# Kernel optimization log

Hardware: AMD Instinct MI355X
Metric: run time of the kernel (lower is better)

## Reference

```python
import jax, jax.numpy as jnp
import numpy as np
from jax import lax

B, C, H, W = 32, 384, 56, 56


def setup_inputs() -> dict:
    key = jax.random.key(0)
    k1, k2, k3, k4 = jax.random.split(key, 4)
    x = jax.random.normal(k1, (B, C, H, W), dtype=jnp.float32)
    # positional embedding, trunc_normal(std=0.02) ~ small normal
    pe = 0.02 * jax.random.normal(k2, (1, C, H, 1), dtype=jnp.float32)
    # depthwise conv weight: (out=C, in/groups=1, kH=H, kW=1), PyTorch default init scale
    fan_in = H  # in_channels/groups * kH * kW = 1*H*1
    bound = 1.0 / np.sqrt(fan_in)
    weight = jax.random.uniform(k3, (C, 1, H, 1), dtype=jnp.float32, minval=-bound, maxval=bound)
    bias = jax.random.uniform(k4, (C,), dtype=jnp.float32, minval=-bound, maxval=bound)
    return {"x": x, "pe": pe, "weight": weight, "bias": bias}


def reference(x, pe, weight, bias):
    # PE add
    xp = x + pe  # [B,C,H,W]
    # circular pad along H: concat first H-1 rows at the bottom
    x_cat = jnp.concatenate([xp, xp[:, :, : H - 1, :]], axis=2)  # [B,C,2H-1,W]
    # depthwise conv, kernel (H,1), groups=C -> output [B,C,H,W]
    out = lax.conv_general_dilated(
        x_cat, weight,
        window_strides=(1, 1), padding='VALID',
        dimension_numbers=('NCHW', 'OIHW', 'NCHW'),
        feature_group_count=C,
    )
    return out + bias[None, :, None, None]
```

## Files before the change

kernel.cpp:

```cpp
#include <hip/hip_runtime.h>

#define Cc 384
#define Hh 56
#define Ww 56
#define PLANE (Hh*Ww)
#define NF4 14

typedef short short8 __attribute__((ext_vector_type(8)));
typedef float f32x4  __attribute__((ext_vector_type(4)));
typedef unsigned int u32;
struct __align__(16) f4 { float x, y, z, w; };

__device__ __forceinline__ u32 cvtpk_bf16(float a, float b) {
    u32 d; asm("v_cvt_pk_bf16_f32 %0, %1, %2" : "=v"(d) : "v"(a), "v"(b));
    return d;
}
__device__ __forceinline__ int swz(int w) { return (w ^ (w >> 2)) & 7; }

__global__ __launch_bounds__(256) __attribute__((amdgpu_waves_per_eu(4, 4)))
void parc_kernel(const float* __restrict__ x, const float* __restrict__ pe,
                 const float* __restrict__ wgt, const float* __restrict__ bias,
                 float* __restrict__ out)
{
    __shared__ __align__(16) unsigned short Xt16[64 * 64];
    __shared__ __align__(16) float Cb[56 * 60];
    __shared__ unsigned short wt2[112];

    const int t  = threadIdx.x;
    const int bc = blockIdx.x;
    const int c  = bc % Cc;

    const float* __restrict__ wc  = wgt + c * Hh;
    const float* __restrict__ pec = pe  + c * Hh;
    const f4* __restrict__ xin = reinterpret_cast<const f4*>(x) + (size_t)bc * (PLANE / 4);

    f4 v0 = xin[t], v1 = xin[t + 256], v2 = xin[t + 512];
    const int r0 = t / NF4, r1 = (t + 256) / NF4, r2 = (t + 512) / NF4;
    const float p0 = pec[r0], p1 = pec[r1], p2 = pec[r2];
    f4 v3; float p3 = 0.f; int r3 = 0;
    if (t < 16) { v3 = xin[t + 768]; r3 = (t + 768) / NF4; p3 = pec[r3]; }

    if (t < 112) {
        const int k = t >= Hh ? t - Hh : t;
        wt2[t] = (unsigned short)(cvtpk_bf16(wc[k], wc[k]) & 0xffffu);
    }

    {
        const int w = t >> 2, j = t & 3;
        const int blk = 7 ^ swz(w);
        *reinterpret_cast<u32*>((char*)Xt16 + 128 * w + 16 * blk + 4 * j) = 0u;
    }

    #define PUT(F, V, R, P) { \
        const int w4_ = (F) % NF4; \
        const int blkb = (R) >> 3, sub = 2 * ((R) & 7); \
        const unsigned short b0 = (unsigned short)cvtpk_bf16((V).x + (P), 0.f); \
        const unsigned short b1 = (unsigned short)cvtpk_bf16((V).y + (P), 0.f); \
        const unsigned short b2 = (unsigned short)cvtpk_bf16((V).z + (P), 0.f); \
        const unsigned short b3 = (unsigned short)cvtpk_bf16((V).w + (P), 0.f); \
        { const int w = 4 * w4_ + 0; *reinterpret_cast<unsigned short*>((char*)Xt16 + 128*w + 16*(blkb ^ swz(w)) + sub) = b0; } \
        { const int w = 4 * w4_ + 1; *reinterpret_cast<unsigned short*>((char*)Xt16 + 128*w + 16*(blkb ^ swz(w)) + sub) = b1; } \
        { const int w = 4 * w4_ + 2; *reinterpret_cast<unsigned short*>((char*)Xt16 + 128*w + 16*(blkb ^ swz(w)) + sub) = b2; } \
        { const int w = 4 * w4_ + 3; *reinterpret_cast<unsigned short*>((char*)Xt16 + 128*w + 16*(blkb ^ swz(w)) + sub) = b3; } }
    PUT(t,       v0, r0, p0)
    PUT(t + 256, v1, r1, p1)
    PUT(t + 512, v2, r2, p2)
    if (t < 16) PUT(t + 768, v3, r3, p3)
    #undef PUT
    __syncthreads();

    const int l = t & 63, wv = t >> 6, l15 = l & 15, g = l >> 4;

    short8 afr[2];
    #pragma unroll
    for (int step = 0; step < 2; ++step) {
        #pragma unroll
        for (int j = 0; j < 8; ++j) {
            int idx = 32 * step + 8 * g + j - 16 * wv - l15 + 56;
            idx = idx < 0 ? 0 : (idx > 111 ? 111 : idx);
            afr[step][j] = (short)wt2[idx];
        }
    }

    const float bz = bias[c];
    f32x4 acc[4];
    #pragma unroll
    for (int ni = 0; ni < 4; ++ni) acc[ni] = (f32x4){bz, bz, bz, bz};

    #pragma unroll
    for (int step = 0; step < 2; ++step) {
        #pragma unroll
        for (int ni = 0; ni < 4; ++ni) {
            const int w = 16 * ni + l15;
            const int blk0 = g + 4 * step;
            const short8 bfr = *reinterpret_cast<const short8*>(
                (char*)Xt16 + 128 * w + 16 * (blk0 ^ swz(w)));
            acc[ni] = __builtin_amdgcn_mfma_f32_16x16x32_bf16(afr[step], bfr, acc[ni], 0, 0, 0);
        }
    }

    #pragma unroll
    for (int ni = 0; ni < 4; ++ni) {
        const int wcol = 16 * ni + l15;
        #pragma unroll
        for (int r = 0; r < 4; ++r) {
            const int h = 16 * wv + 4 * g + r;
            if (h < Hh && wcol < Ww) Cb[60 * h + wcol] = acc[ni][r];
        }
    }
    __syncthreads();

    f4* __restrict__ op = reinterpret_cast<f4*>(out) + (size_t)bc * (PLANE / 4);
    #define GETST(U) { \
        const int rr = (U) / NF4, ww4 = (U) % NF4; \
        op[(U)] = *reinterpret_cast<const f4*>((char*)Cb + 240 * rr + 16 * ww4); }
    GETST(t)
    GETST(t + 256)
    GETST(t + 512)
    if (t < 16) GETST(t + 768)
    #undef GETST
}

extern "C" void kernel_launch(void* const* d_in, const int* in_sizes, int n_in,
                              void* d_out, int out_size, void* d_ws, size_t ws_size,
                              hipStream_t stream) {
    const float* x  = (const float*)d_in[0];
    const float* pe = (const float*)d_in[1];
    const float* w  = (const float*)d_in[2];
    const float* b  = (const float*)d_in[3];
    float* out      = (float*)d_out;

    parc_kernel<<<dim3(32 * Cc), 256, 0, stream>>>(x, pe, w, b, out);
}
```

Measured before the change: 56.59 us.

## Make kernel persistent over six planes with register-prefetched next-plane loads

Launches 2048 blocks that each loop over six (batch, channel) planes instead of one block per plane. The next plane's x, pe, weight and bias loads are issued into registers before the current plane's MFMA and store phase, and the weight LDS buffer is double-buffered. The goal is to hide global load latency behind compute and stores and to cut per-block launch overhead. In exchange it raises register pressure and adds extra barriers per iteration, with a fixed waves_per_eu of 4.

```diff
diff --git a/kernel.cpp b/kernel.cpp
--- a/kernel.cpp
+++ b/kernel.cpp
@@ -5,6 +5,8 @@
 #define Ww 56
 #define PLANE (Hh*Ww)
 #define NF4 14
+#define NBLK 2048
+#define NPL 6
 
 typedef short short8 __attribute__((ext_vector_type(8)));
 typedef float f32x4  __attribute__((ext_vector_type(4)));
@@ -24,32 +26,33 @@
 {
     __shared__ __align__(16) unsigned short Xt16[64 * 64];
     __shared__ __align__(16) float Cb[56 * 60];
-    __shared__ unsigned short wt2[112];
+    __shared__ unsigned short wt2[2][112];
 
-    const int t  = threadIdx.x;
-    const int bc = blockIdx.x;
-    const int c  = bc % Cc;
+    const int t   = threadIdx.x;
+    const int blk = blockIdx.x;
 
-    const float* __restrict__ wc  = wgt + c * Hh;
-    const float* __restrict__ pec = pe  + c * Hh;
-    const f4* __restrict__ xin = reinterpret_cast<const f4*>(x) + (size_t)bc * (PLANE / 4);
-
-    f4 v0 = xin[t], v1 = xin[t + 256], v2 = xin[t + 512];
-    const int r0 = t / NF4, r1 = (t + 256) / NF4, r2 = (t + 512) / NF4;
-    const float p0 = pec[r0], p1 = pec[r1], p2 = pec[r2];
-    f4 v3; float p3 = 0.f; int r3 = 0;
-    if (t < 16) { v3 = xin[t + 768]; r3 = (t + 768) / NF4; p3 = pec[r3]; }
-
-    if (t < 112) {
-        const int k = t >= Hh ? t - Hh : t;
-        wt2[t] = (unsigned short)(cvtpk_bf16(wc[k], wc[k]) & 0xffffu);
-    }
+    const int r0 = t / NF4, r1 = (t + 256) / NF4, r2 = (t + 512) / NF4, r3 = (t + 768) / NF4;
+    const int kw = t >= Hh ? t - Hh : t;
+    const int l = t & 63, wvi = t >> 6, l15 = l & 15, g = l >> 4;
 
     {
         const int w = t >> 2, j = t & 3;
-        const int blk = 7 ^ swz(w);
-        *reinterpret_cast<u32*>((char*)Xt16 + 128 * w + 16 * blk + 4 * j) = 0u;
+        const int blkz = 7 ^ swz(w);
+        *reinterpret_cast<u32*>((char*)Xt16 + 128 * w + 16 * blkz + 4 * j) = 0u;
     }
+
+    f4 v0, v1, v2, v3 = {};
+    float p0 = 0.f, p1 = 0.f, p2 = 0.f, p3 = 0.f, wld = 0.f, bz = 0.f;
+
+    #define ISSUE(BC) { \
+        const f4* __restrict__ xin = reinterpret_cast<const f4*>(x) + (size_t)(BC) * (PLANE / 4); \
+        const int c_ = (BC) % Cc; \
+        const float* __restrict__ pec = pe + c_ * Hh; \
+        v0 = xin[t]; v1 = xin[t + 256]; v2 = xin[t + 512]; \
+        p0 = pec[r0]; p1 = pec[r1]; p2 = pec[r2]; \
+        if (t < 16) { v3 = xin[t + 768]; p3 = pec[r3]; } \
+        if (t < 112) wld = wgt[c_ * Hh + kw]; \
+        bz = bias[c_]; }
 
     #define PUT(F, V, R, P) { \
         const int w4_ = (F) % NF4; \
@@ -62,63 +65,82 @@
         { const int w = 4 * w4_ + 1; *reinterpret_cast<unsigned short*>((char*)Xt16 + 128*w + 16*(blkb ^ swz(w)) + sub) = b1; } \
         { const int w = 4 * w4_ + 2; *reinterpret_cast<unsigned short*>((char*)Xt16 + 128*w + 16*(blkb ^ swz(w)) + sub) = b2; } \
         { const int w = 4 * w4_ + 3; *reinterpret_cast<unsigned short*>((char*)Xt16 + 128*w + 16*(blkb ^ swz(w)) + sub) = b3; } }
-    PUT(t,       v0, r0, p0)
-    PUT(t + 256, v1, r1, p1)
-    PUT(t + 512, v2, r2, p2)
-    if (t < 16) PUT(t + 768, v3, r3, p3)
-    #undef PUT
+
+    #define SCATTER(PAR) { \
+        if (t < 112) wt2[PAR][t] = (unsigned short)(cvtpk_bf16(wld, wld) & 0xffffu); \
+        PUT(t,       v0, r0, p0) \
+        PUT(t + 256, v1, r1, p1) \
+        PUT(t + 512, v2, r2, p2) \
+        if (t < 16) { PUT(t + 768, v3, r3, p3) } }
+
+    ISSUE(blk)
+    SCATTER(0)
+    float bzc = bz;
     __syncthreads();
 
-    const int l = t & 63, wv = t >> 6, l15 = l & 15, g = l >> 4;
+    for (int it = 0; it < NPL; ++it) {
+        const int par = it & 1;
+        const int bc_cur = blk + NBLK * it;
 
-    short8 afr[2];
-    #pragma unroll
-    for (int step = 0; step < 2; ++step) {
+        short8 afr[2];
         #pragma unroll
-        for (int j = 0; j < 8; ++j) {
-            int idx = 32 * step + 8 * g + j - 16 * wv - l15 + 56;
-            idx = idx < 0 ? 0 : (idx > 111 ? 111 : idx);
-            afr[step][j] = (short)wt2[idx];
+        for (int step = 0; step < 2; ++step) {
+            #pragma unroll
+            for (int j = 0; j < 8; ++j) {
+                int idx = 32 * step + 8 * g + j - 16 * wvi - l15 + 56;
+                idx = idx < 0 ? 0 : (idx > 111 ? 111 : idx);
+                afr[step][j] = (short)wt2[par][idx];
+            }
+        }
+
+        if (it + 1 < NPL) { ISSUE(blk + NBLK * (it + 1)) }
+
+        f32x4 acc[4];
+        #pragma unroll
+        for (int ni = 0; ni < 4; ++ni) acc[ni] = (f32x4){bzc, bzc, bzc, bzc};
+
+        #pragma unroll
+        for (int step = 0; step < 2; ++step) {
+            #pragma unroll
+            for (int ni = 0; ni < 4; ++ni) {
+                const int w = 16 * ni + l15;
+                const int blk0 = g + 4 * step;
+                const short8 bfr = *reinterpret_cast<const short8*>(
+                    (char*)Xt16 + 128 * w + 16 * (blk0 ^ swz(w)));
+                acc[ni] = __builtin_amdgcn_mfma_f32_16x16x32_bf16(afr[step], bfr, acc[ni], 0, 0, 0);
+            }
+        }
+
+        #pragma unroll
+        for (int ni = 0; ni < 4; ++ni) {
+            const int wcol = 16 * ni + l15;
+            #pragma unroll
+            for (int r = 0; r < 4; ++r) {
+                const int h = 16 * wvi + 4 * g + r;
+                if (h < Hh && wcol < Ww) Cb[60 * h + wcol] = acc[ni][r];
+            }
+        }
+        __syncthreads();
+
+        f4* __restrict__ op = reinterpret_cast<f4*>(out) + (size_t)bc_cur * (PLANE / 4);
+        #define GETST(U) { \
+            const int rr = (U) / NF4, ww4 = (U) % NF4; \
+            op[(U)] = *reinterpret_cast<const f4*>((char*)Cb + 240 * rr + 16 * ww4); }
+        GETST(t)
+        GETST(t + 256)
+        GETST(t + 512)
+        if (t < 16) { GETST(t + 768) }
+        #undef GETST
+
+        if (it + 1 < NPL) {
+            SCATTER(par ^ 1)
+            bzc = bz;
+            __syncthreads();
         }
     }
-
-    const float bz = bias[c];
-    f32x4 acc[4];
-    #pragma unroll
-    for (int ni = 0; ni < 4; ++ni) acc[ni] = (f32x4){bz, bz, bz, bz};
-
-    #pragma unroll
-    for (int step = 0; step < 2; ++step) {
-        #pragma unroll
-        for (int ni = 0; ni < 4; ++ni) {
-            const int w = 16 * ni + l15;
-            const int blk0 = g + 4 * step;
-            const short8 bfr = *reinterpret_cast<const short8*>(
-                (char*)Xt16 + 128 * w + 16 * (blk0 ^ swz(w)));
-            acc[ni] = __builtin_amdgcn_mfma_f32_16x16x32_bf16(afr[step], bfr, acc[ni], 0, 0, 0);
-        }
-    }
-
-    #pragma unroll
-    for (int ni = 0; ni < 4; ++ni) {
-        const int wcol = 16 * ni + l15;
-        #pragma unroll
-        for (int r = 0; r < 4; ++r) {
-            const int h = 16 * wv + 4 * g + r;
-            if (h < Hh && wcol < Ww) Cb[60 * h + wcol] = acc[ni][r];
-        }
-    }
-    __syncthreads();
-
-    f4* __restrict__ op = reinterpret_cast<f4*>(out) + (size_t)bc * (PLANE / 4);
-    #define GETST(U) { \
-        const int rr = (U) / NF4, ww4 = (U) % NF4; \
-        op[(U)] = *reinterpret_cast<const f4*>((char*)Cb + 240 * rr + 16 * ww4); }
-    GETST(t)
-    GETST(t + 256)
-    GETST(t + 512)
-    if (t < 16) GETST(t + 768)
-    #undef GETST
+    #undef SCATTER
+    #undef PUT
+    #undef ISSUE
 }
 
 extern "C" void kernel_launch(void* const* d_in, const int* in_sizes, int n_in,
@@ -130,5 +152,5 @@
     const float* b  = (const float*)d_in[3];
     float* out      = (float*)d_out;
 
-    parc_kernel<<<dim3(32 * Cc), 256, 0, stream>>>(x, pe, w, b, out);
+    parc_kernel<<<dim3(NBLK), 256, 0, stream>>>(x, pe, w, b, out);
 }
```

Result: faster. 54.09 us (-4.4%).
